# Kernel optimization log

Hardware: AMD Instinct MI355X
Metric: run time of the kernel (lower is better)

Reference implementation:

```python
import jax, jax.numpy as jnp
import numpy as np

B, C, H, W, E, R, TOP_K = 8, 128, 128, 128, 4, 64, 2


def setup_inputs() -> dict:
    key = jax.random.key(0)
    ks = jax.random.split(key, 12)
    s = 0.02
    return {
        "x": jax.random.normal(ks[0], (B, C, H, W), jnp.float32),
        "shared": jax.random.normal(ks[1], (B, C, H, W), jnp.float32),
        # FrequencyEmbedding MLP: Linear(C,2C) -> GELU -> Linear(2C,C)
        "mlp_w1": jax.random.normal(ks[2], (C, 2 * C), jnp.float32) * s,
        "mlp_b1": jnp.zeros((2 * C,), jnp.float32),
        "mlp_w2": jax.random.normal(ks[3], (2 * C, C), jnp.float32) * s,
        "mlp_b2": jnp.zeros((C,), jnp.float32),
        # routing gates: Linear(C,E) on pooled x, Linear(C,E) on freq emb
        "gate_w": jax.random.normal(ks[4], (C, E), jnp.float32) * s,
        "freq_gate_w": jax.random.normal(ks[5], (C, E), jnp.float32) * s,
        # per-expert 1x1 conv weights (ModExpert.proj, expert_layer=Identity)
        "exp_w0": jax.random.normal(ks[6], (E, R, C), jnp.float32) * s,  # dim->rank
        "exp_w1": jax.random.normal(ks[7], (E, R, C), jnp.float32) * s,  # dim->rank (on shared)
        "exp_w2": jax.random.normal(ks[8], (E, C, R), jnp.float32) * s,  # rank->dim
        # AdapterLayer.proj_out 1x1 conv
        "proj_w": jax.random.normal(ks[9], (C, C), jnp.float32) * s,
    }


def reference(x, shared, mlp_w1, mlp_b1, mlp_w2, mlp_b2, gate_w, freq_gate_w,
              exp_w0, exp_w1, exp_w2, proj_w):
    b, c = x.shape[0], x.shape[1]
    # --- FrequencyEmbedding: frozen depthwise high-pass 3x3 -> GELU -> mean(HW) -> MLP ---
    hp = jnp.array([[-1., -1., -1.], [-1., 8., -1.], [-1., -1., -1.]], dtype=x.dtype)
    kern = jnp.broadcast_to(hp, (c, 1, 3, 3))
    h = jax.lax.conv_general_dilated(
        x, kern, window_strides=(1, 1), padding='SAME',
        feature_group_count=c, dimension_numbers=('NCHW', 'OIHW', 'NCHW'))
    h = jax.nn.gelu(h, approximate=False)
    fe = h.mean(axis=(-2, -1))                                    # [B, C]
    fe = jax.nn.gelu(fe @ mlp_w1 + mlp_b1, approximate=False) @ mlp_w2 + mlp_b2
    # --- RoutingFunction (eval / noiseless): softmax -> top-k -> scatter gates ---
    pooled = x.mean(axis=(-2, -1))                                # [B, C]
    logits = pooled @ gate_w + fe @ freq_gate_w                   # [B, E]
    scores = jax.nn.softmax(logits, axis=-1)
    vals, idx = jax.lax.top_k(scores, TOP_K)
    gates = jnp.zeros_like(scores).at[jnp.arange(b)[:, None], idx].set(vals)  # [B, E]
    # --- Experts (dense equivalent of SparseDispatcher gather->expert->scatter-add) ---
    # expert_e(x, shared) = x + W2_e @ ((W0_e @ x) * silu(W1_e @ shared))
    a = jnp.einsum('bchw,erc->berhw', x, exp_w0)                  # [B,E,R,H,W]
    g = jax.nn.silu(jnp.einsum('bchw,erc->berhw', shared, exp_w1))
    y = jnp.einsum('berhw,edr->bedhw', a * g, exp_w2)             # [B,E,C,H,W]
    # gated combine; residual shortcut enters once per selected expert, weighted by gate
    out = jnp.einsum('be,bedhw->bdhw', gates, y) + gates.sum(axis=1)[:, None, None, None] * x
    # --- proj_out 1x1 ---
    return jnp.einsum('bchw,dc->bdhw', out, proj_w)
```

## Files before the change

### kernel.cpp

```cpp
#include <hip/hip_runtime.h>
#include <hip/hip_bf16.h>
#include <math.h>

#define CC   128
#define HWN  16384
#define EE   4
#define RR   64
#define TP   64
#define NT   (HWN / TP)

typedef __attribute__((ext_vector_type(8))) short short8;
typedef __attribute__((ext_vector_type(4))) float f32x4;

__device__ __forceinline__ unsigned short f2bf(float f) {
    __hip_bfloat16 h = __float2bfloat16(f);
    return *reinterpret_cast<unsigned short*>(&h);
}
__device__ __forceinline__ float gelu_exact(float v) {
    return 0.5f * v * (1.0f + erff(v * 0.7071067811865475f));
}
__device__ __forceinline__ float silu_f(float v) {
    return v / (1.0f + expf(-v));
}

#define IMS 129
#define PREP_CONV 1024
#define PREP_WCV  (PREP_CONV + 128)
#define PREP_WF   (PREP_WCV + 128)
#define PREP_SHW  (PREP_WF + 512)
#define PREP_MLW  (PREP_SHW + 48)
__global__ __launch_bounds__(256) void k_prep(
    const float* __restrict__ x,   const float* __restrict__ sh,
    const float* __restrict__ proj,
    const float* __restrict__ ew0, const float* __restrict__ ew1,
    const float* __restrict__ ew2,
    const float* __restrict__ mw1, const float* __restrict__ mw2,
    const float* __restrict__ gw,  const float* __restrict__ fgw,
    float* __restrict__ fe0, float* __restrict__ pooled,
    unsigned short* __restrict__ projb, unsigned short* __restrict__ w0b,
    unsigned short* __restrict__ w1b,   unsigned short* __restrict__ w2pb,
    float* __restrict__ dummy)
{
    __shared__ float img[129 * IMS];
    __shared__ float wred[8];
    const int bx = blockIdx.x, tid = threadIdx.x;

    if (bx < PREP_CONV) {
        const int bc = bx;
        const float4* g = (const float4*)(x + (size_t)bc * HWN);
        for (int i = tid; i < HWN / 4; i += 256) {
            const int r = i >> 5, cq = (i & 31) << 2;
            float4 v = g[i];
            float* d = img + r * IMS + cq;
            d[0] = v.x; d[1] = v.y; d[2] = v.z; d[3] = v.w;
        }
        for (int i = tid; i < IMS; i += 256) img[128 * IMS + i] = 0.f;
        __syncthreads();

        const int r  = tid >> 1;
        const int c0 = (tid & 1) << 6;
        const float* pm  = img + r * IMS + c0;
        const float* pt_ = img + ((r > 0)   ? (r - 1) : 128) * IMS + c0;
        const float* pb_ = img + ((r < 127) ? (r + 1) : 128) * IMS + c0;
        float l0, l1, l2, m0, m1, m2;
        if (c0 == 0) { l0 = l1 = l2 = 0.f; }
        else         { l0 = pt_[-1]; l1 = pm[-1]; l2 = pb_[-1]; }
        m0 = pt_[0]; m1 = pm[0]; m2 = pb_[0];
        float sg = 0.f, sx = 0.f;
        #pragma unroll 7
        for (int j = 0; j < 63; ++j) {
            float n0 = pt_[j + 1], n1 = pm[j + 1], n2 = pb_[j + 1];
            float s8 = ((l0 + l1 + l2) + (m0 + m2)) + ((n0 + n1) + n2);
            sg += gelu_exact(8.f * m1 - s8);
            sx += m1;
            l0 = m0; l1 = m1; l2 = m2; m0 = n0; m1 = n1; m2 = n2;
        }
        {
            float n0, n1, n2;
            if (c0 == 64) { n0 = n1 = n2 = 0.f; }
            else          { n0 = pt_[64]; n1 = pm[64]; n2 = pb_[64]; }
            float s8 = ((l0 + l1 + l2) + (m0 + m2)) + ((n0 + n1) + n2);
            sg += gelu_exact(8.f * m1 - s8);
            sx += m1;
        }
        for (int off = 32; off > 0; off >>= 1) {
            sg += __shfl_down(sg, off, 64);
            sx += __shfl_down(sx, off, 64);
        }
        if ((tid & 63) == 0) { wred[tid >> 6] = sg; wred[4 + (tid >> 6)] = sx; }
        __syncthreads();
        if (tid == 0) {
            fe0[bc]    = (wred[0] + wred[1] + wred[2] + wred[3]) * (1.f / 16384.f);
            pooled[bc] = (wred[4] + wred[5] + wred[6] + wred[7]) * (1.f / 16384.f);
        }
    } else if (bx < PREP_WCV) {
        int i = (bx - PREP_CONV) * 256 + tid;
        if (i < CC * CC) projb[i] = f2bf(proj[i]);
        w0b[i] = f2bf(ew0[i]);
        w1b[i] = f2bf(ew1[i]);
    } else if (bx < PREP_WF) {
        const int bb = bx - PREP_WCV;
        const int e  = bb >> 5;
        const int d  = ((bb & 31) << 2) + (tid >> 6);
        const int r  = tid & 63;
        const float* pr = proj + d * CC;
        const float* wz = ew2 + (size_t)e * CC * RR + r;
        float a0 = 0.f, a1 = 0.f, a2 = 0.f, a3 = 0.f;
        for (int c = 0; c < CC; c += 4) {
            a0 += pr[c + 0] * wz[(c + 0) * RR];
            a1 += pr[c + 1] * wz[(c + 1) * RR];
            a2 += pr[c + 2] * wz[(c + 2) * RR];
            a3 += pr[c + 3] * wz[(c + 3) * RR];
        }
        w2pb[(e * CC + d) * RR + r] = f2bf((a0 + a1) + (a2 + a3));
    } else if (bx < PREP_SHW) {
        const int wb = bx - PREP_WF;
        const float4* s4 = (const float4*)sh + (size_t)wb * 8192;
        float s = 0.f;
        #pragma unroll 4
        for (int j = 0; j < 32; ++j) {
            float4 v = s4[j * 256 + tid];
            s += (v.x + v.y) + (v.z + v.w);
        }
        if (s == 12345.678f) dummy[0] = s;
    } else {
        const int i = (bx - PREP_SHW) * 256 + tid;
        float s = 0.f;
        for (int j = i; j < CC * 2 * CC; j += 48 * 256) s += mw1[j] + mw2[j];
        if (i < CC * EE) s += gw[i] + fgw[i];
        if (s == 12345.678f) dummy[1] = s;
    }
}

__global__ __launch_bounds__(256) void k_route(
    const float* __restrict__ fe0, const float* __restrict__ pooled,
    const float* __restrict__ w1, const float* __restrict__ b1,
    const float* __restrict__ w2, const float* __restrict__ b2,
    const float* __restrict__ gw, const float* __restrict__ fgw,
    float* __restrict__ gates, float* __restrict__ gsum)
{
    const int b = blockIdx.x, tid = threadIdx.x;
    __shared__ float hh[256];
    __shared__ float fe[128];
    __shared__ float lg[4];
    {
        const float* f0 = fe0 + b * CC;
        float a[8];
        #pragma unroll
        for (int j = 0; j < 8; ++j) a[j] = 0.f;
        for (int c = 0; c < CC; c += 8)
            #pragma unroll
            for (int j = 0; j < 8; ++j) a[j] += f0[c + j] * w1[(c + j) * 256 + tid];
        float acc = b1[tid] + ((a[0]+a[1]) + (a[2]+a[3])) + ((a[4]+a[5]) + (a[6]+a[7]));
        hh[tid] = gelu_exact(acc);
    }
    __syncthreads();
    if (tid < 128) {
        float a[8];
        #pragma unroll
        for (int j = 0; j < 8; ++j) a[j] = 0.f;
        for (int c = 0; c < 256; c += 8)
            #pragma unroll
            for (int j = 0; j < 8; ++j) a[j] += hh[c + j] * w2[(c + j) * 128 + tid];
        fe[tid] = b2[tid] + ((a[0]+a[1]) + (a[2]+a[3])) + ((a[4]+a[5]) + (a[6]+a[7]));
    }
    __syncthreads();
    if (tid < EE) {
        const float* pl = pooled + b * CC;
        float l0=0.f, l1=0.f, l2=0.f, l3=0.f;
        for (int c = 0; c < CC; c += 4) {
            l0 += pl[c+0] * gw[(c+0) * EE + tid] + fe[c+0] * fgw[(c+0) * EE + tid];
            l1 += pl[c+1] * gw[(c+1) * EE + tid] + fe[c+1] * fgw[(c+1) * EE + tid];
            l2 += pl[c+2] * gw[(c+2) * EE + tid] + fe[c+2] * fgw[(c+2) * EE + tid];
            l3 += pl[c+3] * gw[(c+3) * EE + tid] + fe[c+3] * fgw[(c+3) * EE + tid];
        }
        lg[tid] = (l0 + l1) + (l2 + l3);
    }
    __syncthreads();
    if (tid == 0) {
        float mx = fmaxf(fmaxf(lg[0], lg[1]), fmaxf(lg[2], lg[3]));
        float sc[EE]; float ssum = 0.f;
        for (int e = 0; e < EE; ++e) { sc[e] = expf(lg[e] - mx); ssum += sc[e]; }
        float inv = 1.f / ssum;
        for (int e = 0; e < EE; ++e) sc[e] *= inv;
        int i1 = 0;
        for (int e = 1; e < EE; ++e) if (sc[e] > sc[i1]) i1 = e;
        int i2 = -1;
        for (int e = 0; e < EE; ++e) {
            if (e == i1) continue;
            if (i2 < 0 || sc[e] > sc[i2]) i2 = e;
        }
        for (int e = 0; e < EE; ++e)
            gates[b * EE + e] = (e == i1) ? sc[i1] : (e == i2 ? sc[i2] : 0.f);
        gsum[b] = sc[i1] + sc[i2];
    }
}

__global__ __launch_bounds__(256, 4) void k_experts(
    const float* __restrict__ x, const float* __restrict__ sh,
    const unsigned short* __restrict__ w0b, const unsigned short* __restrict__ w1b,
    const unsigned short* __restrict__ w2pb, const unsigned short* __restrict__ projb,
    const float* __restrict__ gates, const float* __restrict__ gsum,
    float* __restrict__ out)
{
    __shared__ __align__(16) unsigned short xs [TP * CC];
    __shared__ __align__(16) unsigned short shs[TP * CC];
    __shared__ __align__(16) unsigned short us [TP * RR];
    const int tid  = threadIdx.x;
    const int b    = blockIdx.x >> 8;
    const int tile = blockIdx.x & (NT - 1);
    const int p0   = tile * TP;

    {
        const int p  = tid & 63;
        const int cb = tid >> 6;
        const float* xp = x  + (size_t)b * CC * HWN + p0 + p;
        const float* sp = sh + (size_t)b * CC * HWN + p0 + p;
        #pragma unroll
        for (int it = 0; it < 4; ++it) {
            const int c0 = it * 32 + cb * 8;
            const int sw = p * CC + (((it * 4 + cb) ^ (p & 15)) << 3);
            unsigned short t0[8], t1[8];
            #pragma unroll
            for (int j = 0; j < 8; ++j) t0[j] = f2bf(xp[(size_t)(c0 + j) * HWN]);
            #pragma unroll
            for (int j = 0; j < 8; ++j) t1[j] = f2bf(sp[(size_t)(c0 + j) * HWN]);
            *(uint4*)&xs [sw] = *(uint4*)t0;
            *(uint4*)&shs[sw] = *(uint4*)t1;
        }
    }
    __syncthreads();

    const int wv = tid >> 6;
    const int ln = tid & 63;
    const int lp = ln & 15;
    const int lq = ln >> 4;

    f32x4 acc[2][4];
    #pragma unroll
    for (int i = 0; i < 2; ++i)
        #pragma unroll
        for (int j = 0; j < 4; ++j) acc[i][j] = (f32x4){0.f, 0.f, 0.f, 0.f};

    {
        const int d0 = wv * 32;
        #pragma unroll
        for (int ks = 0; ks < 4; ++ks) {
            const int k0 = ks * 32 + lq * 8;
            const int ch = ks * 4 + lq;
            short8 a0 = *(const short8*)&projb[(d0 +      lp) * CC + k0];
            short8 a1 = *(const short8*)&projb[(d0 + 16 + lp) * CC + k0];
            #pragma unroll
            for (int pt = 0; pt < 4; ++pt) {
                short8 bf = *(const short8*)&xs[(pt * 16 + lp) * CC + ((ch ^ lp) << 3)];
                acc[0][pt] = __builtin_amdgcn_mfma_f32_16x16x32_bf16(a0, bf, acc[0][pt], 0, 0, 0);
                acc[1][pt] = __builtin_amdgcn_mfma_f32_16x16x32_bf16(a1, bf, acc[1][pt], 0, 0, 0);
            }
        }
        const float gs = gsum[b];
        #pragma unroll
        for (int i = 0; i < 2; ++i)
            #pragma unroll
            for (int j = 0; j < 4; ++j) acc[i][j] *= gs;
    }

    for (int e = 0; e < EE; ++e) {
        const float ge = gates[b * EE + e];
        if (ge == 0.f) continue;

        f32x4 af[4], gf[4];
        #pragma unroll
        for (int pt = 0; pt < 4; ++pt) { af[pt] = (f32x4){0.f,0.f,0.f,0.f}; gf[pt] = (f32x4){0.f,0.f,0.f,0.f}; }
        const unsigned short* w0e = w0b + (size_t)(e * RR + wv * 16) * CC;
        const unsigned short* w1e = w1b + (size_t)(e * RR + wv * 16) * CC;
        #pragma unroll
        for (int ks = 0; ks < 4; ++ks) {
            const int k0 = ks * 32 + lq * 8;
            const int ch = ks * 4 + lq;
            short8 a0 = *(const short8*)&w0e[lp * CC + k0];
            short8 a1 = *(const short8*)&w1e[lp * CC + k0];
            #pragma unroll
            for (int pt = 0; pt < 4; ++pt) {
                const int sw = (pt * 16 + lp) * CC + ((ch ^ lp) << 3);
                short8 bx = *(const short8*)&xs [sw];
                short8 bs = *(const short8*)&shs[sw];
                af[pt] = __builtin_amdgcn_mfma_f32_16x16x32_bf16(a0, bx, af[pt], 0, 0, 0);
                gf[pt] = __builtin_amdgcn_mfma_f32_16x16x32_bf16(a1, bs, gf[pt], 0, 0, 0);
            }
        }
        __syncthreads();
        #pragma unroll
        for (int pt = 0; pt < 4; ++pt) {
            unsigned short t[4];
            #pragma unroll
            for (int i = 0; i < 4; ++i)
                t[i] = f2bf(ge * af[pt][i] * silu_f(gf[pt][i]));
            const int p = pt * 16 + lp;
            const int addr = p * RR + (((wv * 2 + (lq >> 1)) ^ (lp & 7)) << 3) + ((lq & 1) << 2);
            *(uint2*)&us[addr] = *(uint2*)t;
        }
        __syncthreads();
        const unsigned short* w2e = w2pb + (size_t)(e * CC + wv * 32) * RR;
        #pragma unroll
        for (int ks = 0; ks < 2; ++ks) {
            const int k0 = ks * 32 + lq * 8;
            const int ch = ks * 4 + lq;
            short8 a0 = *(const short8*)&w2e[lp * RR + k0];
            short8 a1 = *(const short8*)&w2e[(16 + lp) * RR + k0];
            #pragma unroll
            for (int pt = 0; pt < 4; ++pt) {
                short8 bu = *(const short8*)&us[(pt * 16 + lp) * RR + ((ch ^ (lp & 7)) << 3)];
                acc[0][pt] = __builtin_amdgcn_mfma_f32_16x16x32_bf16(a0, bu, acc[0][pt], 0, 0, 0);
                acc[1][pt] = __builtin_amdgcn_mfma_f32_16x16x32_bf16(a1, bu, acc[1][pt], 0, 0, 0);
            }
        }
    }

    {
        const int d0 = wv * 32;
        #pragma unroll
        for (int dt = 0; dt < 2; ++dt)
            #pragma unroll
            for (int pt = 0; pt < 4; ++pt) {
                float* ob = out + ((size_t)(b * CC + d0 + dt * 16 + lq * 4)) * HWN + p0 + pt * 16 + lp;
                #pragma unroll
                for (int i = 0; i < 4; ++i)
                    ob[(size_t)i * HWN] = acc[dt][pt][i];
            }
    }
}

extern "C" void kernel_launch(void* const* d_in, const int* in_sizes, int n_in,
                              void* d_out, int out_size, void* d_ws, size_t ws_size,
                              hipStream_t stream) {
    const float* x    = (const float*)d_in[0];
    const float* shr  = (const float*)d_in[1];
    const float* mw1  = (const float*)d_in[2];
    const float* mb1  = (const float*)d_in[3];
    const float* mw2  = (const float*)d_in[4];
    const float* mb2  = (const float*)d_in[5];
    const float* gw   = (const float*)d_in[6];
    const float* fgw  = (const float*)d_in[7];
    const float* ew0  = (const float*)d_in[8];
    const float* ew1  = (const float*)d_in[9];
    const float* ew2  = (const float*)d_in[10];
    const float* pw   = (const float*)d_in[11];
    float* out = (float*)d_out;

    float* ws     = (float*)d_ws;
    float* fe0    = ws + 0;
    float* pooled = ws + 1024;
    float* gates  = ws + 2048;
    float* gsum   = ws + 2080;
    float* dummy  = ws + 2088;
    unsigned short* projb = (unsigned short*)(ws + 2112);
    unsigned short* w0b   = projb + 16384;
    unsigned short* w1b   = w0b + 32768;
    unsigned short* w2pb  = w1b + 32768;

    k_prep   <<<PREP_MLW, 256, 0, stream>>>(x, shr, pw, ew0, ew1, ew2, mw1, mw2,
                                            gw, fgw, fe0, pooled, projb, w0b, w1b, w2pb, dummy);
    k_route  <<<8,        256, 0, stream>>>(fe0, pooled, mw1, mb1, mw2, mb2, gw, fgw, gates, gsum);
    k_experts<<<8 * NT,   256, 0, stream>>>(x, shr, w0b, w1b, w2pb, projb, gates, gsum, out);
}
```

Baseline: 261.2 us.

## Pre-pack x and shared to bf16 pairs in output buffer; drop LDS stencil staging

The prep kernel now converts x and shared into channel-pair packed bf16 words and writes them into the output buffer as scratch. The expert kernel then reads 32-bit packed words instead of doing strided fp32 loads plus per-element conversion. This halves the bytes the expert kernel loads and removes its conversion work. The high-pass conv blocks now read rows straight from global memory with float4 loads instead of staging the whole image in LDS. The old dummy read of shared, which only warmed the cache, is replaced by the real conversion pass. The cost is an extra full write and re-read of the packed data, and the expert kernel's in-place overwrite of out depends on each tile reading only its own pixels before writing them.

```diff
diff --git a/kernel.cpp b/kernel.cpp
--- a/kernel.cpp
+++ b/kernel.cpp
@@ -16,6 +16,9 @@
     __hip_bfloat16 h = __float2bfloat16(f);
     return *reinterpret_cast<unsigned short*>(&h);
 }
+__device__ __forceinline__ unsigned pk2bf(float lo, float hi) {
+    return (unsigned)f2bf(lo) | ((unsigned)f2bf(hi) << 16);
+}
 __device__ __forceinline__ float gelu_exact(float v) {
     return 0.5f * v * (1.0f + erff(v * 0.7071067811865475f));
 }
@@ -23,12 +26,11 @@
     return v / (1.0f + expf(-v));
 }
 
-#define IMS 129
 #define PREP_CONV 1024
 #define PREP_WCV  (PREP_CONV + 128)
 #define PREP_WF   (PREP_WCV + 128)
-#define PREP_SHW  (PREP_WF + 512)
-#define PREP_MLW  (PREP_SHW + 48)
+#define PREP_TR   (PREP_WF + 1024)
+#define PREP_GRID (PREP_TR + 48)
 __global__ __launch_bounds__(256) void k_prep(
     const float* __restrict__ x,   const float* __restrict__ sh,
     const float* __restrict__ proj,
@@ -39,49 +41,50 @@
     float* __restrict__ fe0, float* __restrict__ pooled,
     unsigned short* __restrict__ projb, unsigned short* __restrict__ w0b,
     unsigned short* __restrict__ w1b,   unsigned short* __restrict__ w2pb,
-    float* __restrict__ dummy)
+    float* __restrict__ outw, float* __restrict__ dummy)
 {
-    __shared__ float img[129 * IMS];
     __shared__ float wred[8];
     const int bx = blockIdx.x, tid = threadIdx.x;
 
     if (bx < PREP_CONV) {
         const int bc = bx;
-        const float4* g = (const float4*)(x + (size_t)bc * HWN);
-        for (int i = tid; i < HWN / 4; i += 256) {
-            const int r = i >> 5, cq = (i & 31) << 2;
-            float4 v = g[i];
-            float* d = img + r * IMS + cq;
-            d[0] = v.x; d[1] = v.y; d[2] = v.z; d[3] = v.w;
-        }
-        for (int i = tid; i < IMS; i += 256) img[128 * IMS + i] = 0.f;
-        __syncthreads();
-
+        const float* base = x + (size_t)bc * HWN;
         const int r  = tid >> 1;
         const int c0 = (tid & 1) << 6;
-        const float* pm  = img + r * IMS + c0;
-        const float* pt_ = img + ((r > 0)   ? (r - 1) : 128) * IMS + c0;
-        const float* pb_ = img + ((r < 127) ? (r + 1) : 128) * IMS + c0;
-        float l0, l1, l2, m0, m1, m2;
-        if (c0 == 0) { l0 = l1 = l2 = 0.f; }
-        else         { l0 = pt_[-1]; l1 = pm[-1]; l2 = pb_[-1]; }
-        m0 = pt_[0]; m1 = pm[0]; m2 = pb_[0];
+        const float* rm = base + r * 128 + c0;
+        const float* rt = rm - 128;
+        const float* rb = rm + 128;
+        const bool hT = (r > 0), hB = (r < 127);
+        float tl, ml, bl;
+        if (c0 == 0) { tl = ml = bl = 0.f; }
+        else         { tl = hT ? rt[-1] : 0.f; ml = rm[-1]; bl = hB ? rb[-1] : 0.f; }
+        float4 tC = hT ? ((const float4*)rt)[0] : (float4){0.f,0.f,0.f,0.f};
+        float4 mC = ((const float4*)rm)[0];
+        float4 bC = hB ? ((const float4*)rb)[0] : (float4){0.f,0.f,0.f,0.f};
         float sg = 0.f, sx = 0.f;
-        #pragma unroll 7
-        for (int j = 0; j < 63; ++j) {
-            float n0 = pt_[j + 1], n1 = pm[j + 1], n2 = pb_[j + 1];
-            float s8 = ((l0 + l1 + l2) + (m0 + m2)) + ((n0 + n1) + n2);
-            sg += gelu_exact(8.f * m1 - s8);
-            sx += m1;
-            l0 = m0; l1 = m1; l2 = m2; m0 = n0; m1 = n1; m2 = n2;
-        }
-        {
-            float n0, n1, n2;
-            if (c0 == 64) { n0 = n1 = n2 = 0.f; }
-            else          { n0 = pt_[64]; n1 = pm[64]; n2 = pb_[64]; }
-            float s8 = ((l0 + l1 + l2) + (m0 + m2)) + ((n0 + n1) + n2);
-            sg += gelu_exact(8.f * m1 - s8);
-            sx += m1;
+        #pragma unroll
+        for (int j = 0; j < 16; ++j) {
+            float4 tN, mN, bN;
+            if (j < 15) {
+                tN = hT ? ((const float4*)rt)[j + 1] : (float4){0.f,0.f,0.f,0.f};
+                mN = ((const float4*)rm)[j + 1];
+                bN = hB ? ((const float4*)rb)[j + 1] : (float4){0.f,0.f,0.f,0.f};
+            } else {
+                float tr_ = 0.f, mr_ = 0.f, br_ = 0.f;
+                if (c0 == 0) { tr_ = hT ? rt[64] : 0.f; mr_ = rm[64]; br_ = hB ? rb[64] : 0.f; }
+                tN = (float4){tr_,0.f,0.f,0.f}; mN = (float4){mr_,0.f,0.f,0.f}; bN = (float4){br_,0.f,0.f,0.f};
+            }
+            const float tA[6] = {tl, tC.x, tC.y, tC.z, tC.w, tN.x};
+            const float mA[6] = {ml, mC.x, mC.y, mC.z, mC.w, mN.x};
+            const float bA[6] = {bl, bC.x, bC.y, bC.z, bC.w, bN.x};
+            #pragma unroll
+            for (int k = 0; k < 4; ++k) {
+                float s8 = ((tA[k] + tA[k+1]) + (tA[k+2] + mA[k]))
+                         + ((mA[k+2] + bA[k]) + (bA[k+1] + bA[k+2]));
+                sg += gelu_exact(8.f * mA[k+1] - s8);
+                sx += mA[k+1];
+            }
+            tl = tC.w; ml = mC.w; bl = bC.w; tC = tN; mC = mN; bC = bN;
         }
         for (int off = 32; off > 0; off >>= 1) {
             sg += __shfl_down(sg, off, 64);
@@ -113,18 +116,27 @@
             a3 += pr[c + 3] * wz[(c + 3) * RR];
         }
         w2pb[(e * CC + d) * RR + r] = f2bf((a0 + a1) + (a2 + a3));
-    } else if (bx < PREP_SHW) {
-        const int wb = bx - PREP_WF;
-        const float4* s4 = (const float4*)sh + (size_t)wb * 8192;
-        float s = 0.f;
-        #pragma unroll 4
-        for (int j = 0; j < 32; ++j) {
-            float4 v = s4[j * 256 + tid];
-            s += (v.x + v.y) + (v.z + v.w);
-        }
-        if (s == 12345.678f) dummy[0] = s;
+    } else if (bx < PREP_TR) {
+        const int idx = bx - PREP_WF;
+        const int d   = idx & 127;
+        const int b   = idx >> 7;
+        const float* s0 = (d < 64)
+            ? x  + ((size_t)b * CC + 2 * d) * HWN
+            : sh + ((size_t)b * CC + 2 * (d - 64)) * HWN;
+        const float4* a4 = (const float4*)s0;
+        const float4* c4 = (const float4*)(s0 + HWN);
+        uint4* dst = (uint4*)((unsigned*)outw + ((size_t)b * CC + d) * HWN);
+        for (int i = tid; i < HWN / 4; i += 256) {
+            float4 a = a4[i], c = c4[i];
+            uint4 w;
+            w.x = pk2bf(a.x, c.x);
+            w.y = pk2bf(a.y, c.y);
+            w.z = pk2bf(a.z, c.z);
+            w.w = pk2bf(a.w, c.w);
+            dst[i] = w;
+        }
     } else {
-        const int i = (bx - PREP_SHW) * 256 + tid;
+        const int i = (bx - PREP_TR) * 256 + tid;
         float s = 0.f;
         for (int j = i; j < CC * 2 * CC; j += 48 * 256) s += mw1[j] + mw2[j];
         if (i < CC * EE) s += gw[i] + fgw[i];
@@ -197,7 +209,6 @@
 }
 
 __global__ __launch_bounds__(256, 4) void k_experts(
-    const float* __restrict__ x, const float* __restrict__ sh,
     const unsigned short* __restrict__ w0b, const unsigned short* __restrict__ w1b,
     const unsigned short* __restrict__ w2pb, const unsigned short* __restrict__ projb,
     const float* __restrict__ gates, const float* __restrict__ gsum,
@@ -212,21 +223,20 @@
     const int p0   = tile * TP;
 
     {
+        const unsigned* wsrc = (const unsigned*)out + ((size_t)b * CC) * HWN + p0;
         const int p  = tid & 63;
-        const int cb = tid >> 6;
-        const float* xp = x  + (size_t)b * CC * HWN + p0 + p;
-        const float* sp = sh + (size_t)b * CC * HWN + p0 + p;
+        const int qh = tid >> 6;
         #pragma unroll
         for (int it = 0; it < 4; ++it) {
-            const int c0 = it * 32 + cb * 8;
-            const int sw = p * CC + (((it * 4 + cb) ^ (p & 15)) << 3);
-            unsigned short t0[8], t1[8];
-            #pragma unroll
-            for (int j = 0; j < 8; ++j) t0[j] = f2bf(xp[(size_t)(c0 + j) * HWN]);
-            #pragma unroll
-            for (int j = 0; j < 8; ++j) t1[j] = f2bf(sp[(size_t)(c0 + j) * HWN]);
-            *(uint4*)&xs [sw] = *(uint4*)t0;
-            *(uint4*)&shs[sw] = *(uint4*)t1;
+            const int q  = it * 4 + qh;
+            const int sw = p * CC + ((q ^ (p & 15)) << 3);
+            const unsigned* px_ = wsrc + (size_t)(q * 4) * HWN + p;
+            const unsigned* ps_ = wsrc + (size_t)(64 + q * 4) * HWN + p;
+            uint4 wx, wh;
+            wx.x = px_[0]; wx.y = px_[HWN]; wx.z = px_[2 * HWN]; wx.w = px_[3 * HWN];
+            wh.x = ps_[0]; wh.y = ps_[HWN]; wh.z = ps_[2 * HWN]; wh.w = ps_[3 * HWN];
+            *(uint4*)&xs [sw] = wx;
+            *(uint4*)&shs[sw] = wh;
         }
     }
     __syncthreads();
@@ -358,8 +368,9 @@
     unsigned short* w1b   = w0b + 32768;
     unsigned short* w2pb  = w1b + 32768;
 
-    k_prep   <<<PREP_MLW, 256, 0, stream>>>(x, shr, pw, ew0, ew1, ew2, mw1, mw2,
-                                            gw, fgw, fe0, pooled, projb, w0b, w1b, w2pb, dummy);
-    k_route  <<<8,        256, 0, stream>>>(fe0, pooled, mw1, mb1, mw2, mb2, gw, fgw, gates, gsum);
-    k_experts<<<8 * NT,   256, 0, stream>>>(x, shr, w0b, w1b, w2pb, projb, gates, gsum, out);
-}
+    k_prep   <<<PREP_GRID, 256, 0, stream>>>(x, shr, pw, ew0, ew1, ew2, mw1, mw2,
+                                             gw, fgw, fe0, pooled, projb, w0b, w1b, w2pb,
+                                             out, dummy);
+    k_route  <<<8,         256, 0, stream>>>(fe0, pooled, mw1, mb1, mw2, mb2, gw, fgw, gates, gsum);
+    k_experts<<<8 * NT,    256, 0, stream>>>(w0b, w1b, w2pb, projb, gates, gsum, out);
+}
```

New measurement: 296.1 us. 13.4% more time.
